# Kernel optimization log

Hardware: AMD Instinct MI355X
Metric: run time of the kernel (lower is better)

The kernel has to match this reference:

```python
import jax, jax.numpy as jnp
import numpy as np

N_NODES = 50000
N_EDGES = 600000
D_FEAT = 128
HIDDEN = 128
OUT = 64


def sage_conv(x, src, dst, Wl, bl, Wr, n_nodes):
    # message = x[src] gathered per edge; mean-aggregated at dst
    msg = x[src]                                            # [E, d]
    agg = jax.ops.segment_sum(msg, dst, num_segments=n_nodes)   # [N, d]
    cnt = jax.ops.segment_sum(jnp.ones((src.shape[0],), x.dtype), dst,
                              num_segments=n_nodes)             # [N]
    mean = agg / jnp.maximum(cnt, 1.0)[:, None]
    # PyG SAGEConv: lin_l(mean_neighbors) + lin_r(x_root); only lin_l has bias
    return mean @ Wl + bl + x @ Wr


def setup_inputs() -> dict:
    key = jax.random.key(0)
    ks = jax.random.split(key, 7)
    x = jax.random.normal(ks[0], (N_NODES, D_FEAT), dtype=jnp.float32)
    edge_index = jax.random.randint(ks[1], (2, N_EDGES), 0, N_NODES, dtype=jnp.int64)
    s1 = 1.0 / np.sqrt(D_FEAT)
    s2 = 1.0 / np.sqrt(HIDDEN)
    W1l = jax.random.normal(ks[2], (D_FEAT, HIDDEN), dtype=jnp.float32) * s1
    b1l = jnp.zeros((HIDDEN,), dtype=jnp.float32)
    W1r = jax.random.normal(ks[3], (D_FEAT, HIDDEN), dtype=jnp.float32) * s1
    W2l = jax.random.normal(ks[4], (HIDDEN, OUT), dtype=jnp.float32) * s2
    b2l = jnp.zeros((OUT,), dtype=jnp.float32)
    W2r = jax.random.normal(ks[5], (HIDDEN, OUT), dtype=jnp.float32) * s2
    return {"x": x, "edge_index": edge_index, "W1l": W1l, "b1l": b1l,
            "W1r": W1r, "W2l": W2l, "b2l": b2l, "W2r": W2r}


def reference(x, edge_index, W1l, b1l, W1r, W2l, b2l, W2r):
    n = x.shape[0]
    src, dst = edge_index[0], edge_index[1]
    h = sage_conv(x, src, dst, W1l, b1l, W1r, n)
    h = jax.nn.relu(h)
    out = sage_conv(h, src, dst, W2l, b2l, W2r, n)
    return out
```

## Files before the change

### kernel.cpp

```cpp
#include <hip/hip_runtime.h>
#include <cstdint>
#include <cstddef>

#define D 128
#define O2 64
#define PAD 136
#define CAP 64

typedef __attribute__((ext_vector_type(8))) short bf16x8;
typedef __attribute__((ext_vector_type(4))) float f32x4;

__device__ inline unsigned short f2bf(float f) {
  union { float f; uint32_t u; } v; v.f = f;
  uint32_t r = v.u + 0x7FFF + ((v.u >> 16) & 1);
  return (unsigned short)(r >> 16);
}
__device__ inline float bf_lo(uint32_t w) {
  union { uint32_t u; float f; } v; v.u = w << 16; return v.f;
}
__device__ inline float bf_hi(uint32_t w) {
  union { uint32_t u; float f; } v; v.u = w & 0xFFFF0000u; return v.f;
}

__global__ __launch_bounds__(256) void prep_all(
    const int* __restrict__ src, const int* __restrict__ dst,
    int* __restrict__ deg, unsigned short* __restrict__ eidx, int n_edges,
    const float* __restrict__ x, const float* __restrict__ W1l,
    const float* __restrict__ W1r, const float* __restrict__ W2l,
    const float* __restrict__ W2r, unsigned short* __restrict__ xb,
    unsigned short* __restrict__ WT1, unsigned short* __restrict__ WT2,
    int n_nodes, int edge_blocks, int xb_blocks)
{
  int b = blockIdx.x;
  if (b < edge_blocks) {
    const int half = n_edges >> 1;
    int e = b * 256 + threadIdx.x;
    if (e < half) {
      int d0 = dst[e],        d1 = dst[e + half];
      int s0 = src[e],        s1 = src[e + half];
      int p0 = atomicAdd(&deg[d0], 1);
      int p1 = atomicAdd(&deg[d1], 1);
      if (p0 < CAP) eidx[(size_t)d0 * CAP + p0] = (unsigned short)s0;
      if (p1 < CAP) eidx[(size_t)d1 * CAP + p1] = (unsigned short)s1;
    }
  } else if (b < edge_blocks + xb_blocks) {
    int i = (b - edge_blocks) * 256 + threadIdx.x;
    if (i < n_nodes * 32) {
      int n = i >> 5, q = i & 31;
      float4 v = ((const float4*)x)[(size_t)n * 32 + q];
      unsigned long long o =
          (unsigned long long)f2bf(v.x)
        | ((unsigned long long)f2bf(v.y) << 16)
        | ((unsigned long long)f2bf(v.z) << 32)
        | ((unsigned long long)f2bf(v.w) << 48);
      *(unsigned long long*)(xb + (size_t)n * 128 + q * 4) = o;
    }
  } else {
    int t = (b - edge_blocks - xb_blocks) * 256 + threadIdx.x;
    if (t < 128 * 256) {
      int n = t >> 8, k = t & 255;
      float w = (k < 128) ? W1l[(size_t)k * 128 + n] : W1r[(size_t)(k - 128) * 128 + n];
      WT1[t] = f2bf(w);
    } else {
      int u = t - 128 * 256;
      if (u < 128 * 128) {
        int n = u >> 7, k = u & 127;
        float w = (n < 64) ? W2l[(size_t)k * 64 + n] : W2r[(size_t)k * 64 + (n - 64)];
        WT2[u] = f2bf(w);
      }
    }
  }
}

__global__ __launch_bounds__(256) void gather1_kernel(
    const unsigned short* __restrict__ xb, const unsigned short* __restrict__ eidx,
    const int* __restrict__ deg, unsigned short* __restrict__ mean, int n_nodes)
{
  const int j = threadIdx.x & 7;
  const int g = threadIdx.x >> 3;
  const int n = blockIdx.x * 32 + g;
  if (n >= n_nodes) return;
  const int dg = deg[n];
  const int cnt = min(dg, CAP);
  const unsigned short* bucket = eidx + (size_t)n * CAP;
  float a[16];
  #pragma unroll
  for (int i = 0; i < 16; i++) a[i] = 0.f;
  int p = 0;
  for (; p + 8 <= cnt; p += 8) {
    uint4 bi = *(const uint4*)(bucket + p);
    int s[8];
    s[0] = bi.x & 0xFFFF; s[1] = bi.x >> 16;
    s[2] = bi.y & 0xFFFF; s[3] = bi.y >> 16;
    s[4] = bi.z & 0xFFFF; s[5] = bi.z >> 16;
    s[6] = bi.w & 0xFFFF; s[7] = bi.w >> 16;
    uint4 v0[8], v1[8];
    #pragma unroll
    for (int q = 0; q < 8; q++) {
      const unsigned short* r = xb + (size_t)s[q] * 128 + j * 16;
      v0[q] = *(const uint4*)r;
      v1[q] = *(const uint4*)(r + 8);
    }
    #pragma unroll
    for (int q = 0; q < 8; q++) {
      a[0]+=bf_lo(v0[q].x); a[1]+=bf_hi(v0[q].x);
      a[2]+=bf_lo(v0[q].y); a[3]+=bf_hi(v0[q].y);
      a[4]+=bf_lo(v0[q].z); a[5]+=bf_hi(v0[q].z);
      a[6]+=bf_lo(v0[q].w); a[7]+=bf_hi(v0[q].w);
      a[8]+=bf_lo(v1[q].x); a[9]+=bf_hi(v1[q].x);
      a[10]+=bf_lo(v1[q].y); a[11]+=bf_hi(v1[q].y);
      a[12]+=bf_lo(v1[q].z); a[13]+=bf_hi(v1[q].z);
      a[14]+=bf_lo(v1[q].w); a[15]+=bf_hi(v1[q].w);
    }
  }
  for (; p + 4 <= cnt; p += 4) {
    uint2 bi = *(const uint2*)(bucket + p);
    int s[4];
    s[0] = bi.x & 0xFFFF; s[1] = bi.x >> 16;
    s[2] = bi.y & 0xFFFF; s[3] = bi.y >> 16;
    uint4 v0[4], v1[4];
    #pragma unroll
    for (int q = 0; q < 4; q++) {
      const unsigned short* r = xb + (size_t)s[q] * 128 + j * 16;
      v0[q] = *(const uint4*)r;
      v1[q] = *(const uint4*)(r + 8);
    }
    #pragma unroll
    for (int q = 0; q < 4; q++) {
      a[0]+=bf_lo(v0[q].x); a[1]+=bf_hi(v0[q].x);
      a[2]+=bf_lo(v0[q].y); a[3]+=bf_hi(v0[q].y);
      a[4]+=bf_lo(v0[q].z); a[5]+=bf_hi(v0[q].z);
      a[6]+=bf_lo(v0[q].w); a[7]+=bf_hi(v0[q].w);
      a[8]+=bf_lo(v1[q].x); a[9]+=bf_hi(v1[q].x);
      a[10]+=bf_lo(v1[q].y); a[11]+=bf_hi(v1[q].y);
      a[12]+=bf_lo(v1[q].z); a[13]+=bf_hi(v1[q].z);
      a[14]+=bf_lo(v1[q].w); a[15]+=bf_hi(v1[q].w);
    }
  }
  for (; p < cnt; p++) {
    const unsigned short* rA = xb + (size_t)bucket[p] * 128 + j * 16;
    uint4 vA0 = *(const uint4*)rA, vA1 = *(const uint4*)(rA + 8);
    a[0]+=bf_lo(vA0.x); a[1]+=bf_hi(vA0.x); a[2]+=bf_lo(vA0.y); a[3]+=bf_hi(vA0.y);
    a[4]+=bf_lo(vA0.z); a[5]+=bf_hi(vA0.z); a[6]+=bf_lo(vA0.w); a[7]+=bf_hi(vA0.w);
    a[8]+=bf_lo(vA1.x); a[9]+=bf_hi(vA1.x); a[10]+=bf_lo(vA1.y); a[11]+=bf_hi(vA1.y);
    a[12]+=bf_lo(vA1.z); a[13]+=bf_hi(vA1.z); a[14]+=bf_lo(vA1.w); a[15]+=bf_hi(vA1.w);
  }
  const float ic = 1.0f / fmaxf((float)dg, 1.0f);
  uint4 o0, o1;
  o0.x = ((uint32_t)f2bf(a[1]*ic) << 16) | f2bf(a[0]*ic);
  o0.y = ((uint32_t)f2bf(a[3]*ic) << 16) | f2bf(a[2]*ic);
  o0.z = ((uint32_t)f2bf(a[5]*ic) << 16) | f2bf(a[4]*ic);
  o0.w = ((uint32_t)f2bf(a[7]*ic) << 16) | f2bf(a[6]*ic);
  o1.x = ((uint32_t)f2bf(a[9]*ic) << 16) | f2bf(a[8]*ic);
  o1.y = ((uint32_t)f2bf(a[11]*ic) << 16) | f2bf(a[10]*ic);
  o1.z = ((uint32_t)f2bf(a[13]*ic) << 16) | f2bf(a[12]*ic);
  o1.w = ((uint32_t)f2bf(a[15]*ic) << 16) | f2bf(a[14]*ic);
  unsigned short* mr = mean + (size_t)n * 128 + j * 16;
  *(uint4*)mr = o0;
  *(uint4*)(mr + 8) = o1;
}

__global__ __launch_bounds__(64, 2) void l12_mfma(
    const unsigned short* __restrict__ mean, const unsigned short* __restrict__ xb,
    const unsigned short* __restrict__ WT1, const unsigned short* __restrict__ WT2,
    const float* __restrict__ b1l, unsigned short* __restrict__ hl,
    float* __restrict__ outp, int n_nodes)
{
  __shared__ unsigned short s_h[32 * PAD];
  const int lane = threadIdx.x;
  const int quad = lane >> 4, l15 = lane & 15;
  const int N0 = blockIdx.x * 32;
  const int ra0 = min(N0 + l15, n_nodes - 1);
  const int ra1 = min(N0 + 16 + l15, n_nodes - 1);

  bf16x8 af[2][8];
  #pragma unroll
  for (int s = 0; s < 4; s++) {
    af[0][s]     = *(const bf16x8*)(mean + (size_t)ra0 * 128 + quad * 8 + s * 32);
    af[1][s]     = *(const bf16x8*)(mean + (size_t)ra1 * 128 + quad * 8 + s * 32);
    af[0][s + 4] = *(const bf16x8*)(xb   + (size_t)ra0 * 128 + quad * 8 + s * 32);
    af[1][s + 4] = *(const bf16x8*)(xb   + (size_t)ra1 * 128 + quad * 8 + s * 32);
  }

  f32x4 acc[2][8];
  #pragma unroll
  for (int rt = 0; rt < 2; rt++)
    #pragma unroll
    for (int tt = 0; tt < 8; tt++) acc[rt][tt] = (f32x4){0.f, 0.f, 0.f, 0.f};

  const unsigned short* b1 = WT1 + (size_t)l15 * 256 + quad * 8;
  bf16x8 cur[8], nxt[8];
  #pragma unroll
  for (int s = 0; s < 8; s++) cur[s] = *(const bf16x8*)(b1 + s * 32);
  #pragma unroll
  for (int tt = 0; tt < 8; tt++) {
    if (tt < 7) {
      #pragma unroll
      for (int s = 0; s < 8; s++)
        nxt[s] = *(const bf16x8*)(b1 + (size_t)(tt + 1) * 16 * 256 + s * 32);
    }
    #pragma unroll
    for (int s = 0; s < 8; s++) {
      acc[0][tt] = __builtin_amdgcn_mfma_f32_16x16x32_bf16(af[0][s], cur[s], acc[0][tt], 0, 0, 0);
      acc[1][tt] = __builtin_amdgcn_mfma_f32_16x16x32_bf16(af[1][s], cur[s], acc[1][tt], 0, 0, 0);
    }
    #pragma unroll
    for (int s = 0; s < 8; s++) cur[s] = nxt[s];
  }

  #pragma unroll
  for (int tt = 0; tt < 8; tt++) {
    int col = tt * 16 + l15;
    float bias = b1l[col];
    #pragma unroll
    for (int rt = 0; rt < 2; rt++) {
      int rb = rt * 16 + quad * 4;
      #pragma unroll
      for (int r = 0; r < 4; r++)
        s_h[(rb + r) * PAD + col] = f2bf(fmaxf(acc[rt][tt][r] + bias, 0.f));
    }
  }
  __syncthreads();

  bf16x8 af2[2][4];
  #pragma unroll
  for (int s = 0; s < 4; s++) {
    af2[0][s] = *(const bf16x8*)(s_h + (l15)      * PAD + quad * 8 + s * 32);
    af2[1][s] = *(const bf16x8*)(s_h + (16 + l15) * PAD + quad * 8 + s * 32);
  }
  f32x4 acc2[2][8];
  #pragma unroll
  for (int rt = 0; rt < 2; rt++)
    #pragma unroll
    for (int tt = 0; tt < 8; tt++) acc2[rt][tt] = (f32x4){0.f, 0.f, 0.f, 0.f};

  const unsigned short* b2 = WT2 + (size_t)l15 * 128 + quad * 8;
  bf16x8 cur2[4], nxt2[4];
  #pragma unroll
  for (int s = 0; s < 4; s++) cur2[s] = *(const bf16x8*)(b2 + s * 32);
  #pragma unroll
  for (int tt = 0; tt < 8; tt++) {
    if (tt < 7) {
      #pragma unroll
      for (int s = 0; s < 4; s++)
        nxt2[s] = *(const bf16x8*)(b2 + (size_t)(tt + 1) * 16 * 128 + s * 32);
    }
    #pragma unroll
    for (int s = 0; s < 4; s++) {
      acc2[0][tt] = __builtin_amdgcn_mfma_f32_16x16x32_bf16(af2[0][s], cur2[s], acc2[0][tt], 0, 0, 0);
      acc2[1][tt] = __builtin_amdgcn_mfma_f32_16x16x32_bf16(af2[1][s], cur2[s], acc2[1][tt], 0, 0, 0);
    }
    #pragma unroll
    for (int s = 0; s < 4; s++) cur2[s] = nxt2[s];
  }

  #pragma unroll
  for (int tt = 0; tt < 8; tt++) {
    int col = tt * 16 + l15;
    #pragma unroll
    for (int rt = 0; rt < 2; rt++) {
      int rowb = N0 + rt * 16 + quad * 4;
      #pragma unroll
      for (int r = 0; r < 4; r++) {
        int row = rowb + r;
        if (row < n_nodes) {
          if (tt < 4) hl[(size_t)row * 64 + col] = f2bf(acc2[rt][tt][r]);
          else        outp[(size_t)row * 64 + (col - 64)] = acc2[rt][tt][r];
        }
      }
    }
  }
}

__global__ __launch_bounds__(256) void gather2_kernel(
    const unsigned short* __restrict__ hl, const unsigned short* __restrict__ eidx,
    const int* __restrict__ deg, const float* __restrict__ b2l,
    float* __restrict__ out, int n_nodes)
{
  const int j = threadIdx.x & 7;
  const int g = threadIdx.x >> 3;
  const int n = blockIdx.x * 32 + g;
  if (n >= n_nodes) return;
  const int dg = deg[n];
  const int cnt = min(dg, CAP);
  const unsigned short* bucket = eidx + (size_t)n * CAP;
  float a[8];
  #pragma unroll
  for (int i = 0; i < 8; i++) a[i] = 0.f;
  int p = 0;
  for (; p + 8 <= cnt; p += 8) {
    uint4 bi = *(const uint4*)(bucket + p);
    int s[8];
    s[0] = bi.x & 0xFFFF; s[1] = bi.x >> 16;
    s[2] = bi.y & 0xFFFF; s[3] = bi.y >> 16;
    s[4] = bi.z & 0xFFFF; s[5] = bi.z >> 16;
    s[6] = bi.w & 0xFFFF; s[7] = bi.w >> 16;
    uint4 v[8];
    #pragma unroll
    for (int q = 0; q < 8; q++)
      v[q] = *(const uint4*)(hl + (size_t)s[q] * 64 + j * 8);
    #pragma unroll
    for (int q = 0; q < 8; q++) {
      a[0]+=bf_lo(v[q].x); a[1]+=bf_hi(v[q].x);
      a[2]+=bf_lo(v[q].y); a[3]+=bf_hi(v[q].y);
      a[4]+=bf_lo(v[q].z); a[5]+=bf_hi(v[q].z);
      a[6]+=bf_lo(v[q].w); a[7]+=bf_hi(v[q].w);
    }
  }
  for (; p + 4 <= cnt; p += 4) {
    uint2 bi = *(const uint2*)(bucket + p);
    int s[4];
    s[0] = bi.x & 0xFFFF; s[1] = bi.x >> 16;
    s[2] = bi.y & 0xFFFF; s[3] = bi.y >> 16;
    uint4 v[4];
    #pragma unroll
    for (int q = 0; q < 4; q++)
      v[q] = *(const uint4*)(hl + (size_t)s[q] * 64 + j * 8);
    #pragma unroll
    for (int q = 0; q < 4; q++) {
      a[0]+=bf_lo(v[q].x); a[1]+=bf_hi(v[q].x);
      a[2]+=bf_lo(v[q].y); a[3]+=bf_hi(v[q].y);
      a[4]+=bf_lo(v[q].z); a[5]+=bf_hi(v[q].z);
      a[6]+=bf_lo(v[q].w); a[7]+=bf_hi(v[q].w);
    }
  }
  for (; p < cnt; p++) {
    uint4 vA = *(const uint4*)(hl + (size_t)bucket[p] * 64 + j * 8);
    a[0]+=bf_lo(vA.x); a[1]+=bf_hi(vA.x); a[2]+=bf_lo(vA.y); a[3]+=bf_hi(vA.y);
    a[4]+=bf_lo(vA.z); a[5]+=bf_hi(vA.z); a[6]+=bf_lo(vA.w); a[7]+=bf_hi(vA.w);
  }
  const float ic = 1.0f / fmaxf((float)dg, 1.0f);
  float* o = out + (size_t)n * 64 + j * 8;
  const float* bb = b2l + j * 8;
  float4 p0 = *(const float4*)(o);
  float4 p1 = *(const float4*)(o + 4);
  p0.x += bb[0] + a[0] * ic; p0.y += bb[1] + a[1] * ic;
  p0.z += bb[2] + a[2] * ic; p0.w += bb[3] + a[3] * ic;
  p1.x += bb[4] + a[4] * ic; p1.y += bb[5] + a[5] * ic;
  p1.z += bb[6] + a[6] * ic; p1.w += bb[7] + a[7] * ic;
  *(float4*)(o) = p0;
  *(float4*)(o + 4) = p1;
}

extern "C" void kernel_launch(void* const* d_in, const int* in_sizes, int n_in,
                              void* d_out, int out_size, void* d_ws, size_t ws_size,
                              hipStream_t stream)
{
  const float* x   = (const float*)d_in[0];
  const int*   ei  = (const int*)d_in[1];
  const float* W1l = (const float*)d_in[2];
  const float* b1l = (const float*)d_in[3];
  const float* W1r = (const float*)d_in[4];
  const float* W2l = (const float*)d_in[5];
  const float* b2l = (const float*)d_in[6];
  const float* W2r = (const float*)d_in[7];
  float* out = (float*)d_out;

  const int n_nodes = in_sizes[0] / D;
  const int n_edges = in_sizes[1] / 2;
  const int* src = ei;
  const int* dst = ei + n_edges;

  char* ws = (char*)d_ws;
  auto align256 = [](size_t v) { return (v + 255) & ~(size_t)255; };
  const size_t szN = align256((size_t)n_nodes * 4);

  size_t o = 0;
  int* deg = (int*)(ws + o);  o += szN;
  unsigned short* eidx = (unsigned short*)(ws + o); o += align256((size_t)n_nodes * CAP * 2);
  unsigned short* WT1  = (unsigned short*)(ws + o); o += align256(128 * 256 * 2);
  unsigned short* WT2  = (unsigned short*)(ws + o); o += align256(128 * 128 * 2);
  unsigned short* xb   = (unsigned short*)(ws + o); o += align256((size_t)n_nodes * 128 * 2);
  unsigned short* mean = (unsigned short*)(ws + o); o += align256((size_t)n_nodes * 128 * 2);
  unsigned short* hl   = (unsigned short*)(ws + o); o += align256((size_t)n_nodes * 64 * 2);

  hipMemsetAsync(deg, 0, szN, stream);

  const int half = n_edges >> 1;
  const int edge_blocks = (half + 255) / 256;
  const int xb_blocks = (n_nodes * 32 + 255) / 256;
  const int w_blocks  = (128 * 256 + 128 * 128 + 255) / 256;

  prep_all<<<edge_blocks + xb_blocks + w_blocks, 256, 0, stream>>>(
      src, dst, deg, eidx, n_edges,
      x, W1l, W1r, W2l, W2r, xb, WT1, WT2, n_nodes, edge_blocks, xb_blocks);

  gather1_kernel<<<(n_nodes + 31) / 32, 256, 0, stream>>>(
      xb, eidx, deg, mean, n_nodes);

  l12_mfma<<<(n_nodes + 31) / 32, 64, 0, stream>>>(
      mean, xb, WT1, WT2, b1l, hl, out, n_nodes);

  gather2_kernel<<<(n_nodes + 31) / 32, 256, 0, stream>>>(
      hl, eidx, deg, b2l, out, n_nodes);
}
```

Before: 187.2 us.

## Sort nodes by degree for gathers and widen gather2 per-thread work

Adds a degree histogram, prefix and scatter pass that builds a node order sorted by (capped) degree. Both gather kernels then walk nodes in that order, so the 8 or 4 lanes of a wave handling different nodes see similar loop trip counts and diverge less. gather2 also switches to 4 lanes per node with 16 features each, raising memory-level parallelism per thread. The cost is three extra small launches, the loss of node-contiguous output writes, and worse locality for the mean/out stores.

```diff
diff --git a/kernel.cpp b/kernel.cpp
--- a/kernel.cpp
+++ b/kernel.cpp
@@ -72,14 +72,60 @@
   }
 }
 
+__global__ __launch_bounds__(256) void hist_kernel(
+    const int* __restrict__ deg, int* __restrict__ hist, int n_nodes)
+{
+  __shared__ int lh[CAP + 1];
+  int t = threadIdx.x;
+  if (t <= CAP) lh[t] = 0;
+  __syncthreads();
+  int n = blockIdx.x * 256 + t;
+  if (n < n_nodes) atomicAdd(&lh[min(deg[n], CAP)], 1);
+  __syncthreads();
+  if (t <= CAP && lh[t]) atomicAdd(&hist[t], lh[t]);
+}
+
+__global__ __launch_bounds__(128) void prefix_kernel(
+    const int* __restrict__ hist, int* __restrict__ base, int* __restrict__ bcnt)
+{
+  if (threadIdx.x == 0) {
+    int acc = 0;
+    for (int b = 0; b <= CAP; b++) { base[b] = acc; acc += hist[b]; }
+  }
+  if (threadIdx.x <= CAP) bcnt[threadIdx.x] = 0;
+}
+
+__global__ __launch_bounds__(256) void scatter_kernel(
+    const int* __restrict__ deg, const int* __restrict__ base, int* __restrict__ bcnt,
+    unsigned short* __restrict__ order, int n_nodes)
+{
+  __shared__ int lh[CAP + 1];
+  __shared__ int lbase[CAP + 1];
+  int t = threadIdx.x;
+  if (t <= CAP) lh[t] = 0;
+  __syncthreads();
+  int n = blockIdx.x * 256 + t;
+  int d = 0, rank = 0;
+  if (n < n_nodes) {
+    d = min(deg[n], CAP);
+    rank = atomicAdd(&lh[d], 1);
+  }
+  __syncthreads();
+  if (t <= CAP && lh[t]) lbase[t] = atomicAdd(&bcnt[t], lh[t]);
+  __syncthreads();
+  if (n < n_nodes) order[base[d] + lbase[d] + rank] = (unsigned short)n;
+}
+
 __global__ __launch_bounds__(256) void gather1_kernel(
     const unsigned short* __restrict__ xb, const unsigned short* __restrict__ eidx,
-    const int* __restrict__ deg, unsigned short* __restrict__ mean, int n_nodes)
+    const int* __restrict__ deg, const unsigned short* __restrict__ order,
+    unsigned short* __restrict__ mean, int n_nodes)
 {
   const int j = threadIdx.x & 7;
   const int g = threadIdx.x >> 3;
-  const int n = blockIdx.x * 32 + g;
-  if (n >= n_nodes) return;
+  const int idx = blockIdx.x * 32 + g;
+  if (idx >= n_nodes) return;
+  const int n = order[idx];
   const int dg = deg[n];
   const int cnt = min(dg, CAP);
   const unsigned short* bucket = eidx + (size_t)n * CAP;
@@ -274,19 +320,20 @@
 
 __global__ __launch_bounds__(256) void gather2_kernel(
     const unsigned short* __restrict__ hl, const unsigned short* __restrict__ eidx,
-    const int* __restrict__ deg, const float* __restrict__ b2l,
-    float* __restrict__ out, int n_nodes)
-{
-  const int j = threadIdx.x & 7;
-  const int g = threadIdx.x >> 3;
-  const int n = blockIdx.x * 32 + g;
-  if (n >= n_nodes) return;
+    const int* __restrict__ deg, const unsigned short* __restrict__ order,
+    const float* __restrict__ b2l, float* __restrict__ out, int n_nodes)
+{
+  const int j = threadIdx.x & 3;
+  const int g = threadIdx.x >> 2;
+  const int idx = blockIdx.x * 64 + g;
+  if (idx >= n_nodes) return;
+  const int n = order[idx];
   const int dg = deg[n];
   const int cnt = min(dg, CAP);
   const unsigned short* bucket = eidx + (size_t)n * CAP;
-  float a[8];
-  #pragma unroll
-  for (int i = 0; i < 8; i++) a[i] = 0.f;
+  float a[16];
+  #pragma unroll
+  for (int i = 0; i < 16; i++) a[i] = 0.f;
   int p = 0;
   for (; p + 8 <= cnt; p += 8) {
     uint4 bi = *(const uint4*)(bucket + p);
@@ -295,16 +342,23 @@
     s[2] = bi.y & 0xFFFF; s[3] = bi.y >> 16;
     s[4] = bi.z & 0xFFFF; s[5] = bi.z >> 16;
     s[6] = bi.w & 0xFFFF; s[7] = bi.w >> 16;
-    uint4 v[8];
-    #pragma unroll
-    for (int q = 0; q < 8; q++)
-      v[q] = *(const uint4*)(hl + (size_t)s[q] * 64 + j * 8);
+    uint4 v0[8], v1[8];
     #pragma unroll
     for (int q = 0; q < 8; q++) {
-      a[0]+=bf_lo(v[q].x); a[1]+=bf_hi(v[q].x);
-      a[2]+=bf_lo(v[q].y); a[3]+=bf_hi(v[q].y);
-      a[4]+=bf_lo(v[q].z); a[5]+=bf_hi(v[q].z);
-      a[6]+=bf_lo(v[q].w); a[7]+=bf_hi(v[q].w);
+      const unsigned short* r = hl + (size_t)s[q] * 64 + j * 16;
+      v0[q] = *(const uint4*)r;
+      v1[q] = *(const uint4*)(r + 8);
+    }
+    #pragma unroll
+    for (int q = 0; q < 8; q++) {
+      a[0]+=bf_lo(v0[q].x); a[1]+=bf_hi(v0[q].x);
+      a[2]+=bf_lo(v0[q].y); a[3]+=bf_hi(v0[q].y);
+      a[4]+=bf_lo(v0[q].z); a[5]+=bf_hi(v0[q].z);
+      a[6]+=bf_lo(v0[q].w); a[7]+=bf_hi(v0[q].w);
+      a[8]+=bf_lo(v1[q].x); a[9]+=bf_hi(v1[q].x);
+      a[10]+=bf_lo(v1[q].y); a[11]+=bf_hi(v1[q].y);
+      a[12]+=bf_lo(v1[q].z); a[13]+=bf_hi(v1[q].z);
+      a[14]+=bf_lo(v1[q].w); a[15]+=bf_hi(v1[q].w);
     }
   }
   for (; p + 4 <= cnt; p += 4) {
@@ -312,34 +366,45 @@
     int s[4];
     s[0] = bi.x & 0xFFFF; s[1] = bi.x >> 16;
     s[2] = bi.y & 0xFFFF; s[3] = bi.y >> 16;
-    uint4 v[4];
-    #pragma unroll
-    for (int q = 0; q < 4; q++)
-      v[q] = *(const uint4*)(hl + (size_t)s[q] * 64 + j * 8);
+    uint4 v0[4], v1[4];
     #pragma unroll
     for (int q = 0; q < 4; q++) {
-      a[0]+=bf_lo(v[q].x); a[1]+=bf_hi(v[q].x);
-      a[2]+=bf_lo(v[q].y); a[3]+=bf_hi(v[q].y);
-      a[4]+=bf_lo(v[q].z); a[5]+=bf_hi(v[q].z);
-      a[6]+=bf_lo(v[q].w); a[7]+=bf_hi(v[q].w);
+      const unsigned short* r = hl + (size_t)s[q] * 64 + j * 16;
+      v0[q] = *(const uint4*)r;
+      v1[q] = *(const uint4*)(r + 8);
+    }
+    #pragma unroll
+    for (int q = 0; q < 4; q++) {
+      a[0]+=bf_lo(v0[q].x); a[1]+=bf_hi(v0[q].x);
+      a[2]+=bf_lo(v0[q].y); a[3]+=bf_hi(v0[q].y);
+      a[4]+=bf_lo(v0[q].z); a[5]+=bf_hi(v0[q].z);
+      a[6]+=bf_lo(v0[q].w); a[7]+=bf_hi(v0[q].w);
+      a[8]+=bf_lo(v1[q].x); a[9]+=bf_hi(v1[q].x);
+      a[10]+=bf_lo(v1[q].y); a[11]+=bf_hi(v1[q].y);
+      a[12]+=bf_lo(v1[q].z); a[13]+=bf_hi(v1[q].z);
+      a[14]+=bf_lo(v1[q].w); a[15]+=bf_hi(v1[q].w);
     }
   }
   for (; p < cnt; p++) {
-    uint4 vA = *(const uint4*)(hl + (size_t)bucket[p] * 64 + j * 8);
-    a[0]+=bf_lo(vA.x); a[1]+=bf_hi(vA.x); a[2]+=bf_lo(vA.y); a[3]+=bf_hi(vA.y);
-    a[4]+=bf_lo(vA.z); a[5]+=bf_hi(vA.z); a[6]+=bf_lo(vA.w); a[7]+=bf_hi(vA.w);
+    const unsigned short* r = hl + (size_t)bucket[p] * 64 + j * 16;
+    uint4 vA0 = *(const uint4*)r, vA1 = *(const uint4*)(r + 8);
+    a[0]+=bf_lo(vA0.x); a[1]+=bf_hi(vA0.x); a[2]+=bf_lo(vA0.y); a[3]+=bf_hi(vA0.y);
+    a[4]+=bf_lo(vA0.z); a[5]+=bf_hi(vA0.z); a[6]+=bf_lo(vA0.w); a[7]+=bf_hi(vA0.w);
+    a[8]+=bf_lo(vA1.x); a[9]+=bf_hi(vA1.x); a[10]+=bf_lo(vA1.y); a[11]+=bf_hi(vA1.y);
+    a[12]+=bf_lo(vA1.z); a[13]+=bf_hi(vA1.z); a[14]+=bf_lo(vA1.w); a[15]+=bf_hi(vA1.w);
   }
   const float ic = 1.0f / fmaxf((float)dg, 1.0f);
-  float* o = out + (size_t)n * 64 + j * 8;
-  const float* bb = b2l + j * 8;
-  float4 p0 = *(const float4*)(o);
-  float4 p1 = *(const float4*)(o + 4);
-  p0.x += bb[0] + a[0] * ic; p0.y += bb[1] + a[1] * ic;
-  p0.z += bb[2] + a[2] * ic; p0.w += bb[3] + a[3] * ic;
-  p1.x += bb[4] + a[4] * ic; p1.y += bb[5] + a[5] * ic;
-  p1.z += bb[6] + a[6] * ic; p1.w += bb[7] + a[7] * ic;
-  *(float4*)(o) = p0;
-  *(float4*)(o + 4) = p1;
+  float* o = out + (size_t)n * 64 + j * 16;
+  const float* bb = b2l + j * 16;
+  #pragma unroll
+  for (int k = 0; k < 4; k++) {
+    float4 pv = *(const float4*)(o + k * 4);
+    pv.x += bb[k*4+0] + a[k*4+0] * ic;
+    pv.y += bb[k*4+1] + a[k*4+1] * ic;
+    pv.z += bb[k*4+2] + a[k*4+2] * ic;
+    pv.w += bb[k*4+3] + a[k*4+3] * ic;
+    *(float4*)(o + k * 4) = pv;
+  }
 }
 
 extern "C" void kernel_launch(void* const* d_in, const int* in_sizes, int n_in,
@@ -366,7 +431,11 @@
   const size_t szN = align256((size_t)n_nodes * 4);
 
   size_t o = 0;
-  int* deg = (int*)(ws + o);  o += szN;
+  int* deg = (int*)(ws + o);   o += szN;
+  int* hist = (int*)(ws + o);  o += 512;
+  int* base = (int*)(ws + o);  o += 512;
+  int* bcnt = (int*)(ws + o);  o += 512;
+  unsigned short* order = (unsigned short*)(ws + o); o += align256((size_t)n_nodes * 2);
   unsigned short* eidx = (unsigned short*)(ws + o); o += align256((size_t)n_nodes * CAP * 2);
   unsigned short* WT1  = (unsigned short*)(ws + o); o += align256(128 * 256 * 2);
   unsigned short* WT2  = (unsigned short*)(ws + o); o += align256(128 * 128 * 2);
@@ -374,23 +443,28 @@
   unsigned short* mean = (unsigned short*)(ws + o); o += align256((size_t)n_nodes * 128 * 2);
   unsigned short* hl   = (unsigned short*)(ws + o); o += align256((size_t)n_nodes * 64 * 2);
 
-  hipMemsetAsync(deg, 0, szN, stream);
+  hipMemsetAsync(deg, 0, szN + 512, stream);
 
   const int half = n_edges >> 1;
   const int edge_blocks = (half + 255) / 256;
   const int xb_blocks = (n_nodes * 32 + 255) / 256;
   const int w_blocks  = (128 * 256 + 128 * 128 + 255) / 256;
+  const int node_blocks = (n_nodes + 255) / 256;
 
   prep_all<<<edge_blocks + xb_blocks + w_blocks, 256, 0, stream>>>(
       src, dst, deg, eidx, n_edges,
       x, W1l, W1r, W2l, W2r, xb, WT1, WT2, n_nodes, edge_blocks, xb_blocks);
 
+  hist_kernel<<<node_blocks, 256, 0, stream>>>(deg, hist, n_nodes);
+  prefix_kernel<<<1, 128, 0, stream>>>(hist, base, bcnt);
+  scatter_kernel<<<node_blocks, 256, 0, stream>>>(deg, base, bcnt, order, n_nodes);
+
   gather1_kernel<<<(n_nodes + 31) / 32, 256, 0, stream>>>(
-      xb, eidx, deg, mean, n_nodes);
+      xb, eidx, deg, order, mean, n_nodes);
 
   l12_mfma<<<(n_nodes + 31) / 32, 64, 0, stream>>>(
       mean, xb, WT1, WT2, b1l, hl, out, n_nodes);
 
-  gather2_kernel<<<(n_nodes + 31) / 32, 256, 0, stream>>>(
-      hl, eidx, deg, b2l, out, n_nodes);
-}
+  gather2_kernel<<<(n_nodes + 63) / 64, 256, 0, stream>>>(
+      hl, eidx, deg, order, b2l, out, n_nodes);
+}
```

Measured after the change: 201.3 us. 1.08x slower.
